# Optimization experiments

Hardware: AMD Instinct MI355X
Metric: run time of the kernel (lower is better)

Reference implementation:

```python
import jax, jax.numpy as jnp
import numpy as np

EPS = 1e-06  # used both as eps and as the F.threshold threshold (mqjs passes eps as th)


def _pair_log_dist_sum(x1, x2, th):
    # dist[i,j] = ||x1_i||^2 + ||x2_j||^2 - 2 x1_i . x2_j  (n x n)
    x1x2 = x1 @ x2.T
    sq1 = jnp.sum(x1 * x1, axis=1)[:, None]
    sq2 = jnp.sum(x2 * x2, axis=1)[None, :]
    dist = sq1 + sq2 - 2.0 * x1x2
    # F.threshold(dist, th, 1): values <= th -> 1; then clamp(min=1), sqrt, log, row-sum
    dist = jnp.where(dist > th, dist, 1.0)
    dist = jnp.maximum(dist, 1.0)
    return jnp.sum(0.5 * jnp.log(dist), axis=1)  # log(sqrt(d)) == 0.5*log(d)


def _mqjs(inp, tgt, eps):
    n = inp.shape[0]
    x1 = inp.reshape(n, -1)
    x2 = tgt.reshape(n, -1)
    p = (x1 + x2) / 2.0
    ce = _pair_log_dist_sum(x1, p, eps) + _pair_log_dist_sum(x2, p, eps)
    se = _pair_log_dist_sum(x1, x1, eps) * (n / (n - 1))
    return jnp.mean(ce - se)


def setup_inputs() -> dict:
    key = jax.random.key(0)
    k1, k2 = jax.random.split(key)
    n, d = 8192, 256
    inp = jax.random.normal(k1, (n, d), dtype=jnp.float32)
    tgt = jax.random.normal(k2, (n, d), dtype=jnp.float32)
    return {"input": inp, "target": tgt}


def reference(input, target):
    return _mqjs(input, target, EPS)
```

## Files before the change

kernel.cpp:

```cpp
#include <hip/hip_runtime.h>

#define N 8192
#define D 256
#define BM 128
#define BJ 64
#define JG 4
#define IG 4
#define GJP (N / (BJ * JG))
#define GIG (N / (BM * IG))
#define NPART (3 * GIG * GJP)

typedef int   i32x4 __attribute__((ext_vector_type(4)));
typedef int   i32x8 __attribute__((ext_vector_type(8)));
typedef float f32x4 __attribute__((ext_vector_type(4)));
typedef float f32x2 __attribute__((ext_vector_type(2)));

__device__ __forceinline__ unsigned pack_fp8x4(float a, float b, float c, float d) {
    unsigned lo = __builtin_amdgcn_cvt_pk_fp8_f32(a, b, 0, false);
    return __builtin_amdgcn_cvt_pk_fp8_f32(c, d, lo, true);
}
__device__ __forceinline__ float dequant_sumsq(unsigned q) {
    const float v0 = __builtin_amdgcn_cvt_f32_fp8(q, 0);
    const float v1 = __builtin_amdgcn_cvt_f32_fp8(q, 1);
    const float v2 = __builtin_amdgcn_cvt_f32_fp8(q, 2);
    const float v3 = __builtin_amdgcn_cvt_f32_fp8(q, 3);
    return fmaf(v0, v0, fmaf(v1, v1, fmaf(v2, v2, v3 * v3)));
}

__global__ void prep_kernel(const float* __restrict__ x1, const float* __restrict__ x2,
                            unsigned* __restrict__ x1q, unsigned* __restrict__ x2q,
                            unsigned* __restrict__ pq,
                            float* __restrict__ sq1, float* __restrict__ sq2,
                            float* __restrict__ sqp) {
    const int tid = threadIdx.x, lane = tid & 63, wv = tid >> 6;
    const int row = blockIdx.x * 4 + wv;
    const size_t eb = (size_t)row * D + lane * 4;
    const float4 a = *(const float4*)(x1 + eb);
    const float4 b = *(const float4*)(x2 + eb);
    const float px = 0.5f * (a.x + b.x), py = 0.5f * (a.y + b.y);
    const float pz = 0.5f * (a.z + b.z), pw = 0.5f * (a.w + b.w);
    const unsigned qa = pack_fp8x4(a.x, a.y, a.z, a.w);
    const unsigned qb = pack_fp8x4(b.x, b.y, b.z, b.w);
    const unsigned qp = pack_fp8x4(px, py, pz, pw);
    const size_t wb = (size_t)row * (D / 4) + lane;
    x1q[wb] = qa; x2q[wb] = qb; pq[wb] = qp;
    float s1 = dequant_sumsq(qa), s2 = dequant_sumsq(qb), sp = dequant_sumsq(qp);
    #pragma unroll
    for (int o = 32; o > 0; o >>= 1) {
        s1 += __shfl_down(s1, o, 64);
        s2 += __shfl_down(s2, o, 64);
        sp += __shfl_down(sp, o, 64);
    }
    if (lane == 0) { sq1[row] = s1; sq2[row] = s2; sqp[row] = sp; }
}

__device__ __forceinline__ f32x4 mfma8(i32x8 a, i32x8 b, f32x4 c) {
    return __builtin_amdgcn_mfma_scale_f32_16x16x128_f8f6f4(
        a, b, c, 0, 0, 0, 0x7F7F7F7F, 0, 0x7F7F7F7F);
}

__device__ __forceinline__ i32x8 frag_at(const unsigned char* b, int olo, int ohi) {
    const i32x4 lo = *(const i32x4*)(b + olo);
    const i32x4 hi = *(const i32x4*)(b + ohi);
    i32x8 f;
    f[0] = lo[0]; f[1] = lo[1]; f[2] = lo[2]; f[3] = lo[3];
    f[4] = hi[0]; f[5] = hi[1]; f[6] = hi[2]; f[7] = hi[3];
    return f;
}

__device__ __forceinline__ void stageB8(const unsigned char* __restrict__ g,
                                        unsigned char* s, int rowbase, size_t kb,
                                        int wv, int srow, int sblk) {
    const int row = wv * 8 + srow;
    __builtin_amdgcn_global_load_lds(
        (const __attribute__((address_space(1))) void*)(g + (size_t)(rowbase + row) * D + kb + sblk * 16),
        (__attribute__((address_space(3))) void*)(s + wv * 1024), 16, 0, 0);
}

__device__ __forceinline__ float logsumP(const f32x4 (&acc)[2][2],
                                         const f32x2 (&sa01)[2], const f32x2 (&sa23)[2],
                                         const float sb[2]) {
    float s = 0.0f;
    #pragma unroll
    for (int ti = 0; ti < 2; ++ti) {
        f32x2 pr = {1.0f, 1.0f};
        #pragma unroll
        for (int tj = 0; tj < 2; ++tj) {
            const f32x2 sbv = {sb[tj], sb[tj]};
            const f32x2 t01 = sa01[ti] + sbv, t23 = sa23[ti] + sbv;
            const f32x2 v01 = {acc[ti][tj][0], acc[ti][tj][1]};
            const f32x2 v23 = {acc[ti][tj][2], acc[ti][tj][3]};
            f32x2 d01 = t01 - 2.0f * v01;
            f32x2 d23 = t23 - 2.0f * v23;
            d01 = __builtin_elementwise_max(d01, (f32x2){1.0f, 1.0f});
            d23 = __builtin_elementwise_max(d23, (f32x2){1.0f, 1.0f});
            pr *= d01; pr *= d23;
        }
        s += __log2f(pr.x * pr.y);
    }
    return s;
}

__device__ __forceinline__ float logsumStraddle(const f32x4 (&acc)[2][2],
                                                const f32x2 (&sa01)[2], const f32x2 (&sa23)[2],
                                                const float sb[2],
                                                int wr, int wc, int quad, int l15,
                                                int I0, int J0) {
    float s = 0.0f;
    #pragma unroll
    for (int ti = 0; ti < 2; ++ti) {
        #pragma unroll
        for (int tj = 0; tj < 2; ++tj) {
            const int j = J0 + wc * 32 + tj * 16 + l15;
            float pr = 1.0f;
            #pragma unroll
            for (int r = 0; r < 4; ++r) {
                const int i = I0 + wr * 32 + ti * 16 + quad * 4 + r;
                const float sav = (r < 2) ? ((r & 1) ? sa01[ti].y : sa01[ti].x)
                                          : ((r & 1) ? sa23[ti].y : sa23[ti].x);
                float d = fmaf(-2.0f, acc[ti][tj][r], sav + sb[tj]);
                d = fmaxf(d, 1.0f);
                const float t = (j > i) ? d : 1.0f;
                const float u = (j >= i) ? d : 1.0f;
                pr *= t * u;
            }
            s += __log2f(pr);
        }
    }
    return s;
}

__global__ __launch_bounds__(512, 4) void mqjs_main(
    const unsigned char* __restrict__ x1q, const unsigned char* __restrict__ x2q,
    const unsigned char* __restrict__ pq,
    const float* __restrict__ sq1, const float* __restrict__ sq2,
    const float* __restrict__ sqp, float* __restrict__ partials) {

    __shared__ __align__(16) unsigned char Bs[JG * 16384];
    __shared__ float red[8];

    const int tid = threadIdx.x;
    const int lane = tid & 63;
    const int wv = tid >> 6;
    const int wr = wv >> 1, wc = wv & 1;
    const int quad = lane >> 4, l15 = lane & 15;
    const int srow = lane >> 3;
    const int sblk = (lane & 7) ^ srow;

    const int z = blockIdx.z;
    const int jbase = blockIdx.x * JG;
    const int Ibase = blockIdx.y * (BM * IG);
    const int pid = (z * GIG + blockIdx.y) * GJP + blockIdx.x;
    const float wse = -(float)N / (float)(N - 1);
    const int Jmax0 = (jbase + JG - 1) * BJ;

    if (z == 2 && Jmax0 < Ibase) {
        if (tid == 0) partials[pid] = 0.0f;
        return;
    }

    const unsigned char* Ag = (z == 1) ? x2q : x1q;
    const unsigned char* Bg = (z == 2) ? x1q : pq;
    const float* sqAg = (z == 1) ? sq2 : sq1;
    const float* sqBg = (z == 2) ? sq1 : sqp;

    #pragma unroll
    for (int jj = 0; jj < JG; ++jj) {
        stageB8(Bg, &Bs[jj * 16384],        (jbase + jj) * BJ, 0,   wv, srow, sblk);
        stageB8(Bg, &Bs[jj * 16384 + 8192], (jbase + jj) * BJ, 128, wv, srow, sblk);
    }

    asm volatile("s_waitcnt vmcnt(0)" ::: "memory");
    __syncthreads();

    const int m0 = wc * 32 + l15;
    const int r7 = m0 & 7;
    const int o0 = m0 * 128 + (((2 * quad)     ^ r7) << 4);
    const int o1 = m0 * 128 + (((2 * quad + 1) ^ r7) << 4);

    float tsum = 0.0f;
    const f32x4 zero4 = {0.0f, 0.0f, 0.0f, 0.0f};

    #pragma unroll 1
    for (int it = 0; it < IG; ++it) {
        const int I0 = Ibase + it * BM;
        if (z == 2 && Jmax0 < I0) continue;

        i32x8 af[2][2];
        f32x2 sa01[2], sa23[2];
        #pragma unroll
        for (int ti = 0; ti < 2; ++ti) {
            #pragma unroll
            for (int kc = 0; kc < 2; ++kc) {
                const size_t ro = (size_t)(I0 + wr * 32 + ti * 16 + l15) * D + kc * 128 + quad * 32;
                af[kc][ti] = *(const i32x8*)(Ag + ro);
            }
            const int sbase = I0 + wr * 32 + ti * 16 + quad * 4;
            const float4 sv = *(const float4*)(sqAg + sbase);
            sa01[ti] = (f32x2){sv.x, sv.y};
            sa23[ti] = (f32x2){sv.z, sv.w};
        }

        #pragma unroll 1
        for (int jj = 0; jj < JG; ++jj) {
            const int J0 = (jbase + jj) * BJ;
            if (z == 2 && J0 < I0) continue;

            const unsigned char* tb = &Bs[jj * 16384];
            const float* sp = sqBg + J0 + m0;
            float sb[2];
            sb[0] = sp[0]; sb[1] = sp[16];

            f32x4 acc[2][2];
            __builtin_amdgcn_s_setprio(1);
            i32x8 b0 = frag_at(tb, o0, o1);
            i32x8 b1 = frag_at(tb + 2048, o0, o1);
            acc[0][0] = mfma8(af[0][0], b0, zero4);
            acc[0][1] = mfma8(af[0][0], b1, zero4);
            acc[1][0] = mfma8(af[0][1], b0, zero4);
            acc[1][1] = mfma8(af[0][1], b1, zero4);
            b0 = frag_at(tb + 8192, o0, o1);
            b1 = frag_at(tb + 8192 + 2048, o0, o1);
            acc[0][0] = mfma8(af[1][0], b0, acc[0][0]);
            acc[0][1] = mfma8(af[1][0], b1, acc[0][1]);
            acc[1][0] = mfma8(af[1][1], b0, acc[1][0]);
            acc[1][1] = mfma8(af[1][1], b1, acc[1][1]);
            __builtin_amdgcn_s_setprio(0);

            if (z < 2) {
                tsum += 0.5f * logsumP(acc, sa01, sa23, sb);
            } else if (J0 >= I0 + BM) {
                tsum += wse * logsumP(acc, sa01, sa23, sb);
            } else {
                tsum += 0.5f * wse * logsumStraddle(acc, sa01, sa23, sb,
                                                    wr, wc, quad, l15, I0, J0);
            }
        }
    }

    tsum *= 0.6931471805599453f;
    #pragma unroll
    for (int o = 32; o > 0; o >>= 1) tsum += __shfl_down(tsum, o, 64);
    if (lane == 0) red[wv] = tsum;
    __syncthreads();
    if (tid == 0) {
        float t = 0.0f;
        #pragma unroll
        for (int i = 0; i < 8; ++i) t += red[i];
        partials[pid] = t;
    }
}

__global__ void finalize_kernel(const float* __restrict__ partials, float* __restrict__ out) {
    const int tid = threadIdx.x;
    const float4 v = ((const float4*)partials)[tid];
    double s = (double)v.x + (double)v.y + (double)v.z + (double)v.w;
    #pragma unroll
    for (int o = 32; o > 0; o >>= 1) s += __shfl_down(s, o, 64);
    __shared__ double r[6];
    if ((tid & 63) == 0) r[tid >> 6] = s;
    __syncthreads();
    if (tid == 0) {
        double t = 0.0;
        #pragma unroll
        for (int i = 0; i < 6; ++i) t += r[i];
        out[0] = (float)(t / (double)N);
    }
}

extern "C" void kernel_launch(void* const* d_in, const int* in_sizes, int n_in,
                              void* d_out, int out_size, void* d_ws, size_t ws_size,
                              hipStream_t stream) {
    const float* x1 = (const float*)d_in[0];
    const float* x2 = (const float*)d_in[1];

    char* ws = (char*)d_ws;
    const size_t MBYTES = (size_t)N * D;
    unsigned* x1q = (unsigned*)(ws);
    unsigned* x2q = (unsigned*)(ws + MBYTES);
    unsigned* pq  = (unsigned*)(ws + 2 * MBYTES);
    float* sq1 = (float*)(ws + 3 * MBYTES);
    float* sq2 = (float*)(ws + 3 * MBYTES + (size_t)N * 4);
    float* sqp = (float*)(ws + 3 * MBYTES + (size_t)N * 8);
    float* partials = (float*)(ws + 3 * MBYTES + (size_t)N * 12);

    prep_kernel<<<N / 4, 256, 0, stream>>>(x1, x2, x1q, x2q, pq, sq1, sq2, sqp);
    mqjs_main<<<dim3(GJP, GIG, 3), 512, 0, stream>>>(
        (const unsigned char*)x1q, (const unsigned char*)x2q, (const unsigned char*)pq,
        sq1, sq2, sqp, partials);
    finalize_kernel<<<1, 384, 0, stream>>>(partials, (float*)d_out);
}
```

Measured before the change: 132.2 us.

## Software-pipeline MFMA tiles with log epilogue for cross-entropy blocks

Splits the main kernel into separate paths for the cross-entropy blocks and the symmetric self-entropy blocks. In the cross-entropy path the four J tiles are fully unrolled with two accumulator sets, so the MFMAs of the next tile are interleaved with the log epilogue of the previous one, guided by sched_group_barrier hints. Launch bounds drop from 4 to 2 waves per SIMD to make room for the extra registers. This adds register pressure and lowers occupancy, and the schedule hints may not match the code the compiler actually emits.

New measurement: 125.0 us. 1.06x faster.

```diff
diff --git a/kernel.cpp b/kernel.cpp
--- a/kernel.cpp
+++ b/kernel.cpp
@@ -130,7 +130,17 @@
     return s;
 }
 
-__global__ __launch_bounds__(512, 4) void mqjs_main(
+__device__ __forceinline__ void sgb_region() {
+    __builtin_amdgcn_sched_group_barrier(0x020, 2, 0);
+    __builtin_amdgcn_sched_group_barrier(0x100, 8, 0);
+    #pragma unroll
+    for (int i = 0; i < 8; ++i) {
+        __builtin_amdgcn_sched_group_barrier(0x008, 1, 0);
+        __builtin_amdgcn_sched_group_barrier(0x002, 6, 0);
+    }
+}
+
+__global__ __launch_bounds__(512, 2) void mqjs_main(
     const unsigned char* __restrict__ x1q, const unsigned char* __restrict__ x2q,
     const unsigned char* __restrict__ pq,
     const float* __restrict__ sq1, const float* __restrict__ sq2,
@@ -181,59 +191,108 @@
     float tsum = 0.0f;
     const f32x4 zero4 = {0.0f, 0.0f, 0.0f, 0.0f};
 
-    #pragma unroll 1
-    for (int it = 0; it < IG; ++it) {
-        const int I0 = Ibase + it * BM;
-        if (z == 2 && Jmax0 < I0) continue;
-
-        i32x8 af[2][2];
-        f32x2 sa01[2], sa23[2];
-        #pragma unroll
-        for (int ti = 0; ti < 2; ++ti) {
+    if (z < 2) {
+        #pragma unroll 1
+        for (int it = 0; it < IG; ++it) {
+            const int I0 = Ibase + it * BM;
+
+            i32x8 af[2][2];
+            f32x2 sa01[2], sa23[2];
             #pragma unroll
-            for (int kc = 0; kc < 2; ++kc) {
-                const size_t ro = (size_t)(I0 + wr * 32 + ti * 16 + l15) * D + kc * 128 + quad * 32;
-                af[kc][ti] = *(const i32x8*)(Ag + ro);
+            for (int ti = 0; ti < 2; ++ti) {
+                #pragma unroll
+                for (int kc = 0; kc < 2; ++kc) {
+                    const size_t ro = (size_t)(I0 + wr * 32 + ti * 16 + l15) * D + kc * 128 + quad * 32;
+                    af[kc][ti] = *(const i32x8*)(Ag + ro);
+                }
+                const int sbase = I0 + wr * 32 + ti * 16 + quad * 4;
+                const float4 sv = *(const float4*)(sqAg + sbase);
+                sa01[ti] = (f32x2){sv.x, sv.y};
+                sa23[ti] = (f32x2){sv.z, sv.w};
             }
-            const int sbase = I0 + wr * 32 + ti * 16 + quad * 4;
-            const float4 sv = *(const float4*)(sqAg + sbase);
-            sa01[ti] = (f32x2){sv.x, sv.y};
-            sa23[ti] = (f32x2){sv.z, sv.w};
+
+            auto TILE = [&](int jj, f32x4 (&acc)[2][2], float (&sb)[2]) {
+                const unsigned char* tb = &Bs[jj * 16384];
+                const float* sp = sqBg + (jbase + jj) * BJ + m0;
+                sb[0] = sp[0]; sb[1] = sp[16];
+                i32x8 b0 = frag_at(tb, o0, o1);
+                i32x8 b1 = frag_at(tb + 2048, o0, o1);
+                acc[0][0] = mfma8(af[0][0], b0, zero4);
+                acc[0][1] = mfma8(af[0][0], b1, zero4);
+                acc[1][0] = mfma8(af[0][1], b0, zero4);
+                acc[1][1] = mfma8(af[0][1], b1, zero4);
+                b0 = frag_at(tb + 8192, o0, o1);
+                b1 = frag_at(tb + 8192 + 2048, o0, o1);
+                acc[0][0] = mfma8(af[1][0], b0, acc[0][0]);
+                acc[0][1] = mfma8(af[1][0], b1, acc[0][1]);
+                acc[1][0] = mfma8(af[1][1], b0, acc[1][0]);
+                acc[1][1] = mfma8(af[1][1], b1, acc[1][1]);
+            };
+            auto EPI = [&](const f32x4 (&acc)[2][2], const float (&sb)[2]) {
+                tsum += 0.5f * logsumP(acc, sa01, sa23, sb);
+            };
+
+            f32x4 accA[2][2], accB[2][2];
+            float sbA[2], sbB[2];
+            TILE(0, accA, sbA);
+            TILE(1, accB, sbB); EPI(accA, sbA); sgb_region();
+            TILE(2, accA, sbA); EPI(accB, sbB); sgb_region();
+            TILE(3, accB, sbB); EPI(accA, sbA); sgb_region();
+            EPI(accB, sbB);
         }
-
+    } else {
         #pragma unroll 1
-        for (int jj = 0; jj < JG; ++jj) {
-            const int J0 = (jbase + jj) * BJ;
-            if (z == 2 && J0 < I0) continue;
-
-            const unsigned char* tb = &Bs[jj * 16384];
-            const float* sp = sqBg + J0 + m0;
-            float sb[2];
-            sb[0] = sp[0]; sb[1] = sp[16];
-
-            f32x4 acc[2][2];
-            __builtin_amdgcn_s_setprio(1);
-            i32x8 b0 = frag_at(tb, o0, o1);
-            i32x8 b1 = frag_at(tb + 2048, o0, o1);
-            acc[0][0] = mfma8(af[0][0], b0, zero4);
-            acc[0][1] = mfma8(af[0][0], b1, zero4);
-            acc[1][0] = mfma8(af[0][1], b0, zero4);
-            acc[1][1] = mfma8(af[0][1], b1, zero4);
-            b0 = frag_at(tb + 8192, o0, o1);
-            b1 = frag_at(tb + 8192 + 2048, o0, o1);
-            acc[0][0] = mfma8(af[1][0], b0, acc[0][0]);
-            acc[0][1] = mfma8(af[1][0], b1, acc[0][1]);
-            acc[1][0] = mfma8(af[1][1], b0, acc[1][0]);
-            acc[1][1] = mfma8(af[1][1], b1, acc[1][1]);
-            __builtin_amdgcn_s_setprio(0);
-
-            if (z < 2) {
-                tsum += 0.5f * logsumP(acc, sa01, sa23, sb);
-            } else if (J0 >= I0 + BM) {
-                tsum += wse * logsumP(acc, sa01, sa23, sb);
-            } else {
-                tsum += 0.5f * wse * logsumStraddle(acc, sa01, sa23, sb,
-                                                    wr, wc, quad, l15, I0, J0);
+        for (int it = 0; it < IG; ++it) {
+            const int I0 = Ibase + it * BM;
+            if (Jmax0 < I0) continue;
+
+            i32x8 af[2][2];
+            f32x2 sa01[2], sa23[2];
+            #pragma unroll
+            for (int ti = 0; ti < 2; ++ti) {
+                #pragma unroll
+                for (int kc = 0; kc < 2; ++kc) {
+                    const size_t ro = (size_t)(I0 + wr * 32 + ti * 16 + l15) * D + kc * 128 + quad * 32;
+                    af[kc][ti] = *(const i32x8*)(Ag + ro);
+                }
+                const int sbase = I0 + wr * 32 + ti * 16 + quad * 4;
+                const float4 sv = *(const float4*)(sqAg + sbase);
+                sa01[ti] = (f32x2){sv.x, sv.y};
+                sa23[ti] = (f32x2){sv.z, sv.w};
+            }
+
+            #pragma unroll 1
+            for (int jj = 0; jj < JG; ++jj) {
+                const int J0 = (jbase + jj) * BJ;
+                if (J0 < I0) continue;
+
+                const unsigned char* tb = &Bs[jj * 16384];
+                const float* sp = sqBg + J0 + m0;
+                float sb[2];
+                sb[0] = sp[0]; sb[1] = sp[16];
+
+                f32x4 acc[2][2];
+                __builtin_amdgcn_s_setprio(1);
+                i32x8 b0 = frag_at(tb, o0, o1);
+                i32x8 b1 = frag_at(tb + 2048, o0, o1);
+                acc[0][0] = mfma8(af[0][0], b0, zero4);
+                acc[0][1] = mfma8(af[0][0], b1, zero4);
+                acc[1][0] = mfma8(af[0][1], b0, zero4);
+                acc[1][1] = mfma8(af[0][1], b1, zero4);
+                b0 = frag_at(tb + 8192, o0, o1);
+                b1 = frag_at(tb + 8192 + 2048, o0, o1);
+                acc[0][0] = mfma8(af[1][0], b0, acc[0][0]);
+                acc[0][1] = mfma8(af[1][0], b1, acc[0][1]);
+                acc[1][0] = mfma8(af[1][1], b0, acc[1][0]);
+                acc[1][1] = mfma8(af[1][1], b1, acc[1][1]);
+                __builtin_amdgcn_s_setprio(0);
+
+                if (J0 >= I0 + BM) {
+                    tsum += wse * logsumP(acc, sa01, sa23, sb);
+                } else {
+                    tsum += 0.5f * wse * logsumStraddle(acc, sa01, sa23, sb,
+                                                        wr, wc, quad, l15, I0, J0);
+                }
             }
         }
     }
```
